# Kernel tuning notes

Hardware: AMD Instinct MI355X
Metric: run time of the kernel (lower is better)

Reference implementation:

```python
import jax, jax.numpy as jnp
import numpy as np
import math

D_MODEL = 1024
N_HEADS = 16
D_K = D_MODEL // N_HEADS
D_FF = 4096
B = 2
S = 2048
LN_EPS = 1e-3  # Keras LayerNormalization default


def setup_inputs() -> dict:
    key = jax.random.key(0)
    ks = jax.random.split(key, 16)
    s = 0.02
    inp = {
        "x": jax.random.normal(ks[0], (B, S, D_MODEL), dtype=jnp.float32),
        "weights": jax.random.uniform(ks[1], (B, S), dtype=jnp.float32),
        # attention projections (Dense: y = x @ W + b)
        "Wq": jax.random.normal(ks[2], (D_MODEL, D_MODEL), jnp.float32) * s,
        "bq": jnp.zeros((D_MODEL,), jnp.float32),
        "Wk": jax.random.normal(ks[3], (D_MODEL, D_MODEL), jnp.float32) * s,
        "bk": jnp.zeros((D_MODEL,), jnp.float32),
        "Wv": jax.random.normal(ks[4], (D_MODEL, D_MODEL), jnp.float32) * s,
        "bv": jnp.zeros((D_MODEL,), jnp.float32),
        "Wo": jax.random.normal(ks[5], (D_MODEL, D_MODEL), jnp.float32) * s,
        "bo": jnp.zeros((D_MODEL,), jnp.float32),
        # FFN
        "W1": jax.random.normal(ks[6], (D_MODEL, D_FF), jnp.float32) * s,
        "b1": jnp.zeros((D_FF,), jnp.float32),
        "W2": jax.random.normal(ks[7], (D_FF, D_MODEL), jnp.float32) * s,
        "b2": jnp.zeros((D_MODEL,), jnp.float32),
        # layer norms
        "g1": jnp.ones((D_MODEL,), jnp.float32),
        "be1": jnp.zeros((D_MODEL,), jnp.float32),
        "g2": jnp.ones((D_MODEL,), jnp.float32),
        "be2": jnp.zeros((D_MODEL,), jnp.float32),
    }
    return inp


def _layer_norm(x, gamma, beta):
    mu = jnp.mean(x, axis=-1, keepdims=True)
    var = jnp.mean(jnp.square(x - mu), axis=-1, keepdims=True)
    return (x - mu) * jax.lax.rsqrt(var + LN_EPS) * gamma + beta


def _block(x, weights, Wq, bq, Wk, bk, Wv, bv, Wo, bo, W1, b1, W2, b2, g1, be1, g2, be2):
    b, s, _ = x.shape
    # projections -> (B, H, S, d_k)
    def split_heads(y):
        return y.reshape(b, s, N_HEADS, D_K).transpose(0, 2, 1, 3)
    Q = split_heads(x @ Wq + bq)
    K = split_heads(x @ Wk + bk)
    V = split_heads(x @ Wv + bv)
    scores = jnp.einsum("bhqd,bhkd->bhqk", Q, K) / math.sqrt(D_K)
    log_w = jnp.log(weights + 1e-20)[:, None, None, :]  # (B,1,1,S)
    attn = jax.nn.softmax(scores + log_w, axis=-1)
    out = jnp.einsum("bhqk,bhkd->bhqd", attn, V)
    out = out.transpose(0, 2, 1, 3).reshape(b, s, D_MODEL)
    attn_out = out @ Wo + bo
    h = _layer_norm(x + attn_out, g1, be1)
    ffn = jax.nn.relu(h @ W1 + b1) @ W2 + b2
    return _layer_norm(h + ffn, g2, be2)


def reference(x, weights, Wq, bq, Wk, bk, Wv, bv, Wo, bo, W1, b1, W2, b2, g1, be1, g2, be2):
    return _block(x, weights, Wq, bq, Wk, bk, Wv, bv, Wo, bo, W1, b1, W2, b2, g1, be1, g2, be2)
```

## Files before the change

kernel.cpp:

```cpp
#include <hip/hip_runtime.h>
#include <cstdint>
#include <cstddef>

#define DM 1024
#define NH 16
#define DKH 64
#define DFF 4096
#define NB 2
#define SQL 2048
#define MROWS (NB * SQL)
#define QKVN 3072

typedef __attribute__((ext_vector_type(8))) __bf16 bf16x8;
typedef __attribute__((ext_vector_type(8))) short short8;
typedef __attribute__((ext_vector_type(4))) float f32x4;

__device__ __forceinline__ unsigned short f2bf(float f) {
    unsigned u = __float_as_uint(f);
    u += 0x7fffu + ((u >> 16) & 1u);
    return (unsigned short)(u >> 16);
}
__device__ __forceinline__ float bf2f(unsigned short u) {
    return __uint_as_float(((unsigned)u) << 16);
}
__device__ __forceinline__ bf16x8 ldfrag(const unsigned short* p) {
    return __builtin_bit_cast(bf16x8, *(const short8*)p);
}
__device__ __forceinline__ void gl_lds16(const void* g, void* lds) {
    __builtin_amdgcn_global_load_lds(
        (const __attribute__((address_space(1))) unsigned int*)g,
        (__attribute__((address_space(3))) unsigned int*)lds, 16, 0, 0);
}
#define MFMA16(a, b, c) __builtin_amdgcn_mfma_f32_16x16x32_bf16(a, b, c, 0, 0, 0)

__global__ __launch_bounds__(256) void cast_f32_bf16(const float* __restrict__ in,
                                                     unsigned short* __restrict__ out, int n) {
    int i = (blockIdx.x * 256 + threadIdx.x) * 4;
    if (i < n) {
        float4 v = *(const float4*)&in[i];
        ushort4 o;
        o.x = f2bf(v.x); o.y = f2bf(v.y); o.z = f2bf(v.z); o.w = f2bf(v.w);
        *(ushort4*)&out[i] = o;
    }
}

__global__ __launch_bounds__(256) void transpose_f32_bf16(const float* __restrict__ in,
                                                          unsigned short* __restrict__ out,
                                                          int K, int N, float scale) {
    __shared__ float tile[32][33];
    const int n0 = blockIdx.x * 32, k0 = blockIdx.y * 32;
    const int tx = threadIdx.x & 31, ty = threadIdx.x >> 5;
#pragma unroll
    for (int i = 0; i < 32; i += 8)
        tile[ty + i][tx] = in[(size_t)(k0 + ty + i) * N + n0 + tx];
    __syncthreads();
#pragma unroll
    for (int i = 0; i < 32; i += 8)
        out[(size_t)(n0 + ty + i) * K + k0 + tx] = f2bf(tile[tx][ty + i] * scale);
}

__global__ __launch_bounds__(256) void vt_transpose(const unsigned short* __restrict__ qkv,
                                                    unsigned short* __restrict__ vt) {
    __shared__ unsigned short tile[32][33];
    const int s0 = blockIdx.x * 32, d0 = blockIdx.y * 32, bh = blockIdx.z;
    const int b = bh >> 4, h = bh & 15;
    const int tx = threadIdx.x & 31, ty = threadIdx.x >> 5;
#pragma unroll
    for (int i = 0; i < 32; i += 8)
        tile[ty + i][tx] = qkv[(size_t)(b * SQL + s0 + ty + i) * QKVN + 2048 + h * DKH + d0 + tx];
    __syncthreads();
#pragma unroll
    for (int i = 0; i < 32; i += 8)
        vt[(size_t)bh * DKH * SQL + (size_t)(d0 + ty + i) * SQL + s0 + tx] = tile[tx][ty + i];
}

__global__ __launch_bounds__(256) void logw_kernel(const float* __restrict__ w,
                                                   float* __restrict__ lw, int n) {
    int i = blockIdx.x * 256 + threadIdx.x;
    if (i < n) lw[i] = logf(w[i] + 1e-20f);
}

__global__ __launch_bounds__(256) void bqkv_kernel(const float* __restrict__ bq,
                                                   const float* __restrict__ bk,
                                                   const float* __restrict__ bv,
                                                   float* __restrict__ out) {
    int i = blockIdx.x * 256 + threadIdx.x;
    if (i < QKVN)
        out[i] = i < 1024 ? bq[i] * 0.125f : (i < 2048 ? bk[i - 1024] : bv[i - 2048]);
}

template <int BN, bool RELU, bool OUT_BF16>
__global__ __launch_bounds__(256) void gemm_kernel(const unsigned short* __restrict__ A,
                                                   const unsigned short* __restrict__ Wt,
                                                   const float* __restrict__ bias,
                                                   void* __restrict__ outp,
                                                   int M, int N, int K) {
    constexpr int NT = BN / 32;
    __shared__ unsigned short As[128 * 64];
    __shared__ unsigned short Bs[BN * 64];
    const int tid = threadIdx.x;
    const int wave = tid >> 6, lane = tid & 63;
    const int col16 = lane & 15, quad = lane >> 4;
    const int lrow = lane >> 3, sblk = (lane & 7) ^ (lrow & 7);
    const int m0 = blockIdx.y * 128, n0 = blockIdx.x * BN;
    const int wm = (wave >> 1) * 64, wn = (wave & 1) * (BN / 2);

    f32x4 acc[4][NT] = {};

    for (int k0 = 0; k0 < K; k0 += 64) {
        __syncthreads();
#pragma unroll
        for (int c = wave; c < 16; c += 4)
            gl_lds16(&A[(size_t)(m0 + c * 8 + lrow) * K + k0 + sblk * 8], &As[c * 512]);
#pragma unroll
        for (int c = wave; c < BN / 8; c += 4)
            gl_lds16(&Wt[(size_t)(n0 + c * 8 + lrow) * K + k0 + sblk * 8], &Bs[c * 512]);
        __syncthreads();
#pragma unroll
        for (int kk8 = 0; kk8 < 8; kk8 += 4) {
            bf16x8 af[4], bfr[NT];
#pragma unroll
            for (int t = 0; t < 4; ++t) {
                int R = wm + t * 16 + col16;
                af[t] = ldfrag(&As[R * 64 + (((kk8 + quad) ^ (R & 7)) << 3)]);
            }
#pragma unroll
            for (int t = 0; t < NT; ++t) {
                int R = wn + t * 16 + col16;
                bfr[t] = ldfrag(&Bs[R * 64 + (((kk8 + quad) ^ (R & 7)) << 3)]);
            }
#pragma unroll
            for (int mt = 0; mt < 4; ++mt)
#pragma unroll
                for (int nt = 0; nt < NT; ++nt)
                    acc[mt][nt] = MFMA16(af[mt], bfr[nt], acc[mt][nt]);
        }
    }

#pragma unroll
    for (int mt = 0; mt < 4; ++mt)
#pragma unroll
        for (int nt = 0; nt < NT; ++nt) {
            int col = n0 + wn + nt * 16 + col16;
            float bv = bias[col];
#pragma unroll
            for (int r = 0; r < 4; ++r) {
                int row = m0 + wm + mt * 16 + quad * 4 + r;
                float v = acc[mt][nt][r] + bv;
                if (RELU) v = fmaxf(v, 0.f);
                if (OUT_BF16)
                    ((unsigned short*)outp)[(size_t)row * N + col] = f2bf(v);
                else
                    ((float*)outp)[(size_t)row * N + col] = v;
            }
        }
}

__global__ __launch_bounds__(256) void flash_kernel(const unsigned short* __restrict__ qkv,
                                                    const unsigned short* __restrict__ vt,
                                                    const float* __restrict__ logw,
                                                    unsigned short* __restrict__ outb) {
    __shared__ unsigned short Ks[64 * 64];
    __shared__ unsigned short Vt[64 * 64];
    __shared__ unsigned short Ps[4][16][72];
    __shared__ float lws[64];

    const int tid = threadIdx.x, wave = tid >> 6, lane = tid & 63;
    const int col16 = lane & 15, quad = lane >> 4;
    const int lrow = lane >> 3, sblk = (lane & 7) ^ (lrow & 7);
    const int bh = blockIdx.y, b = bh >> 4, h = bh & 15;
    const int q0 = blockIdx.x * 64;

    const unsigned short* Kg = qkv + (size_t)b * SQL * QKVN + 1024 + h * DKH;
    const unsigned short* Vg = vt + (size_t)bh * DKH * SQL;

    bf16x8 qf[2];
    {
        const unsigned short* qrow = qkv + (size_t)(b * SQL + q0 + wave * 16 + col16) * QKVN + h * DKH;
        qf[0] = ldfrag(qrow + quad * 8);
        qf[1] = ldfrag(qrow + 32 + quad * 8);
    }
    bf16x8 ones;
    {
        short8 o8 = {0x3f80, 0x3f80, 0x3f80, 0x3f80, 0x3f80, 0x3f80, 0x3f80, 0x3f80};
        ones = __builtin_bit_cast(bf16x8, o8);
    }

    f32x4 o[4] = {};
    f32x4 lacc = {};

    for (int kt = 0; kt < SQL; kt += 64) {
        __syncthreads();
#pragma unroll
        for (int c = wave; c < 8; c += 4) {
            gl_lds16(&Kg[(size_t)(kt + c * 8 + lrow) * QKVN + sblk * 8], &Ks[c * 512]);
            gl_lds16(&Vg[(size_t)(c * 8 + lrow) * SQL + kt + sblk * 8], &Vt[c * 512]);
        }
        if (tid < 64) lws[tid] = logw[b * SQL + kt + tid];
        __syncthreads();

        float pv[4][4];
#pragma unroll
        for (int nt = 0; nt < 4; ++nt) {
            int R = nt * 16 + col16;
            f32x4 s4 = {};
            s4 = MFMA16(qf[0], ldfrag(&Ks[R * 64 + ((quad ^ (R & 7)) << 3)]), s4);
            s4 = MFMA16(qf[1], ldfrag(&Ks[R * 64 + (((4 + quad) ^ (R & 7)) << 3)]), s4);
            float lw = lws[R];
#pragma unroll
            for (int r = 0; r < 4; ++r) pv[nt][r] = __expf(s4[r] + lw);
        }
#pragma unroll
        for (int nt = 0; nt < 4; ++nt)
#pragma unroll
            for (int r = 0; r < 4; ++r)
                Ps[wave][quad * 4 + r][nt * 16 + col16] = f2bf(pv[nt][r]);
        __syncthreads();

#pragma unroll
        for (int kk8 = 0; kk8 < 8; kk8 += 4) {
            bf16x8 psf = ldfrag(&Ps[wave][col16][(kk8 + quad) << 3]);
            lacc = MFMA16(ones, psf, lacc);
#pragma unroll
            for (int dt = 0; dt < 4; ++dt) {
                int R = dt * 16 + col16;
                bf16x8 vf = ldfrag(&Vt[R * 64 + (((kk8 + quad) ^ (R & 7)) << 3)]);
                o[dt] = MFMA16(vf, psf, o[dt]);
            }
        }
    }

    const float rl = 1.0f / lacc[0];
    const int qrow = b * SQL + q0 + wave * 16 + col16;
#pragma unroll
    for (int dt = 0; dt < 4; ++dt) {
        ushort4 h4;
        h4.x = f2bf(o[dt][0] * rl);
        h4.y = f2bf(o[dt][1] * rl);
        h4.z = f2bf(o[dt][2] * rl);
        h4.w = f2bf(o[dt][3] * rl);
        *(ushort4*)&outb[(size_t)qrow * DM + h * DKH + dt * 16 + quad * 4] = h4;
    }
}

__global__ __launch_bounds__(256) void ln1_kernel(const float* __restrict__ x,
                                                  const float* __restrict__ delta,
                                                  const float* __restrict__ g,
                                                  const float* __restrict__ be,
                                                  float* __restrict__ hf,
                                                  unsigned short* __restrict__ hb) {
    const int row = blockIdx.x, tid = threadIdx.x;
    float4 xv = *(const float4*)&x[(size_t)row * DM + tid * 4];
    float4 dv = *(const float4*)&delta[(size_t)row * DM + tid * 4];
    float v[4] = {xv.x + dv.x, xv.y + dv.y, xv.z + dv.z, xv.w + dv.w};
    float s = v[0] + v[1] + v[2] + v[3];
    float ss = v[0] * v[0] + v[1] * v[1] + v[2] * v[2] + v[3] * v[3];
#pragma unroll
    for (int m = 1; m < 64; m <<= 1) { s += __shfl_xor(s, m); ss += __shfl_xor(ss, m); }
    __shared__ float sb[4], ssb[4];
    if ((tid & 63) == 0) { sb[tid >> 6] = s; ssb[tid >> 6] = ss; }
    __syncthreads();
    s = sb[0] + sb[1] + sb[2] + sb[3];
    ss = ssb[0] + ssb[1] + ssb[2] + ssb[3];
    float mu = s * (1.f / DM);
    float var = fmaxf(ss * (1.f / DM) - mu * mu, 0.f);
    float rs = rsqrtf(var + 1e-3f);
#pragma unroll
    for (int i = 0; i < 4; ++i) {
        int c = tid * 4 + i;
        float y = (v[i] - mu) * rs * g[c] + be[c];
        hf[(size_t)row * DM + c] = y;
        hb[(size_t)row * DM + c] = f2bf(y);
    }
}

__global__ __launch_bounds__(256) void ln2_kernel(const float* __restrict__ hf,
                                                  const float* __restrict__ delta,
                                                  const float* __restrict__ g,
                                                  const float* __restrict__ be,
                                                  float* __restrict__ outp) {
    const int row = blockIdx.x, tid = threadIdx.x;
    float4 hv = *(const float4*)&hf[(size_t)row * DM + tid * 4];
    float4 dv = *(const float4*)&delta[(size_t)row * DM + tid * 4];
    float v[4] = {hv.x + dv.x, hv.y + dv.y, hv.z + dv.z, hv.w + dv.w};
    float s = v[0] + v[1] + v[2] + v[3];
    float ss = v[0] * v[0] + v[1] * v[1] + v[2] * v[2] + v[3] * v[3];
#pragma unroll
    for (int m = 1; m < 64; m <<= 1) { s += __shfl_xor(s, m); ss += __shfl_xor(ss, m); }
    __shared__ float sb[4], ssb[4];
    if ((tid & 63) == 0) { sb[tid >> 6] = s; ssb[tid >> 6] = ss; }
    __syncthreads();
    s = sb[0] + sb[1] + sb[2] + sb[3];
    ss = ssb[0] + ssb[1] + ssb[2] + ssb[3];
    float mu = s * (1.f / DM);
    float var = fmaxf(ss * (1.f / DM) - mu * mu, 0.f);
    float rs = rsqrtf(var + 1e-3f);
    float4 ov;
    ov.x = (v[0] - mu) * rs * g[tid * 4 + 0] + be[tid * 4 + 0];
    ov.y = (v[1] - mu) * rs * g[tid * 4 + 1] + be[tid * 4 + 1];
    ov.z = (v[2] - mu) * rs * g[tid * 4 + 2] + be[tid * 4 + 2];
    ov.w = (v[3] - mu) * rs * g[tid * 4 + 3] + be[tid * 4 + 3];
    *(float4*)&outp[(size_t)row * DM + tid * 4] = ov;
}

extern "C" void kernel_launch(void* const* d_in, const int* in_sizes, int n_in,
                              void* d_out, int out_size, void* d_ws, size_t ws_size,
                              hipStream_t stream) {
    const float* x   = (const float*)d_in[0];
    const float* wts = (const float*)d_in[1];
    const float* Wq  = (const float*)d_in[2];
    const float* bq  = (const float*)d_in[3];
    const float* Wk  = (const float*)d_in[4];
    const float* bk  = (const float*)d_in[5];
    const float* Wv  = (const float*)d_in[6];
    const float* bv  = (const float*)d_in[7];
    const float* Wo  = (const float*)d_in[8];
    const float* bo  = (const float*)d_in[9];
    const float* W1  = (const float*)d_in[10];
    const float* b1  = (const float*)d_in[11];
    const float* W2  = (const float*)d_in[12];
    const float* b2  = (const float*)d_in[13];
    const float* g1  = (const float*)d_in[14];
    const float* be1 = (const float*)d_in[15];
    const float* g2  = (const float*)d_in[16];
    const float* be2 = (const float*)d_in[17];

    char* ws = (char*)d_ws;
    const size_t MB = 1u << 20;
    unsigned short* qkv_bf  = (unsigned short*)(ws + 0 * MB);
    unsigned short* vt      = (unsigned short*)(ws + 24 * MB);
    float* attnproj         = (float*)(ws + 0 * MB);
    unsigned short* ffn1_bf = (unsigned short*)(ws + 0 * MB);
    unsigned short* x_bf    = (unsigned short*)(ws + 32 * MB);
    unsigned short* wqkv_t  = (unsigned short*)(ws + 40 * MB);
    unsigned short* Wo_t    = (unsigned short*)(ws + 46 * MB);
    unsigned short* W1_t    = (unsigned short*)(ws + 48 * MB);
    unsigned short* W2_t    = (unsigned short*)(ws + 56 * MB);
    float* ffn2             = (float*)(ws + 32 * MB);
    unsigned short* attn_bf = (unsigned short*)(ws + 64 * MB);
    float* h_f32            = (float*)(ws + 72 * MB);
    unsigned short* h_bf    = (unsigned short*)(ws + 88 * MB);
    float* bqkv             = (float*)(ws + 96 * MB);
    float* logw             = (float*)(ws + 96 * MB + 16384);

    cast_f32_bf16<<<(MROWS * DM) / 1024, 256, 0, stream>>>(x, x_bf, MROWS * DM);
    transpose_f32_bf16<<<dim3(32, 32), 256, 0, stream>>>(Wq, wqkv_t, DM, DM, 0.125f);
    transpose_f32_bf16<<<dim3(32, 32), 256, 0, stream>>>(Wk, wqkv_t + (size_t)1024 * DM, DM, DM, 1.f);
    transpose_f32_bf16<<<dim3(32, 32), 256, 0, stream>>>(Wv, wqkv_t + (size_t)2048 * DM, DM, DM, 1.f);
    transpose_f32_bf16<<<dim3(32, 32), 256, 0, stream>>>(Wo, Wo_t, DM, DM, 1.f);
    transpose_f32_bf16<<<dim3(128, 32), 256, 0, stream>>>(W1, W1_t, DM, DFF, 1.f);
    transpose_f32_bf16<<<dim3(32, 128), 256, 0, stream>>>(W2, W2_t, DFF, DM, 1.f);
    bqkv_kernel<<<12, 256, 0, stream>>>(bq, bk, bv, bqkv);
    logw_kernel<<<(MROWS + 255) / 256, 256, 0, stream>>>(wts, logw, MROWS);

    gemm_kernel<128, false, true><<<dim3(QKVN / 128, MROWS / 128), 256, 0, stream>>>(
        x_bf, wqkv_t, bqkv, qkv_bf, MROWS, QKVN, DM);

    vt_transpose<<<dim3(SQL / 32, DKH / 32, NB * NH), 256, 0, stream>>>(qkv_bf, vt);
    flash_kernel<<<dim3(SQL / 64, NB * NH), 256, 0, stream>>>(qkv_bf, vt, logw, attn_bf);

    gemm_kernel<64, false, false><<<dim3(DM / 64, MROWS / 128), 256, 0, stream>>>(
        attn_bf, Wo_t, bo, attnproj, MROWS, DM, DM);
    ln1_kernel<<<MROWS, 256, 0, stream>>>(x, attnproj, g1, be1, h_f32, h_bf);

    gemm_kernel<128, true, true><<<dim3(DFF / 128, MROWS / 128), 256, 0, stream>>>(
        h_bf, W1_t, b1, ffn1_bf, MROWS, DFF, DM);
    gemm_kernel<64, false, false><<<dim3(DM / 64, MROWS / 128), 256, 0, stream>>>(
        ffn1_bf, W2_t, b2, ffn2, MROWS, DM, DFF);
    ln2_kernel<<<MROWS, 256, 0, stream>>>(h_f32, ffn2, g2, be2, (float*)d_out);
}
```

Baseline: 398.8 us.

## Split attention KV range and narrow GEMMs along K to raise occupancy

The flash attention kernel now splits each query tile's key range into two halves as separate blocks. It writes unnormalized fp32 partial outputs and row sums, which a new combine kernel adds and normalizes into bf16. The Wo and W2 GEMMs (N=1024) now use a 2-way split-K. Each split writes its own fp32 partial buffer, and the LayerNorm kernels add both partials. The goal is more blocks on a GPU with many CUs. The cost is extra memory traffic for the partial buffers, one more kernel launch, and a workspace rearrangement that moves the W2 transpose later.

```diff
diff --git a/kernel.cpp b/kernel.cpp
--- a/kernel.cpp
+++ b/kernel.cpp
@@ -89,7 +89,7 @@
         out[i] = i < 1024 ? bq[i] * 0.125f : (i < 2048 ? bk[i - 1024] : bv[i - 2048]);
 }
 
-template <int BN, bool RELU, bool OUT_BF16>
+template <int BN, bool RELU, bool OUT_BF16, int KSPL>
 __global__ __launch_bounds__(256) void gemm_kernel(const unsigned short* __restrict__ A,
                                                    const unsigned short* __restrict__ Wt,
                                                    const float* __restrict__ bias,
@@ -104,10 +104,12 @@
     const int lrow = lane >> 3, sblk = (lane & 7) ^ (lrow & 7);
     const int m0 = blockIdx.y * 128, n0 = blockIdx.x * BN;
     const int wm = (wave >> 1) * 64, wn = (wave & 1) * (BN / 2);
+    const int kbeg = (KSPL > 1) ? blockIdx.z * (K / KSPL) : 0;
+    const int kend = kbeg + K / KSPL;
 
     f32x4 acc[4][NT] = {};
 
-    for (int k0 = 0; k0 < K; k0 += 64) {
+    for (int k0 = kbeg; k0 < kend; k0 += 64) {
         __syncthreads();
 #pragma unroll
         for (int c = wave; c < 16; c += 4)
@@ -137,12 +139,13 @@
         }
     }
 
+    float* outf = (float*)outp + ((KSPL > 1) ? (size_t)blockIdx.z * M * N : 0);
 #pragma unroll
     for (int mt = 0; mt < 4; ++mt)
 #pragma unroll
         for (int nt = 0; nt < NT; ++nt) {
             int col = n0 + wn + nt * 16 + col16;
-            float bv = bias[col];
+            float bv = (KSPL == 1 || blockIdx.z == 0) ? bias[col] : 0.f;
 #pragma unroll
             for (int r = 0; r < 4; ++r) {
                 int row = m0 + wm + mt * 16 + quad * 4 + r;
@@ -151,7 +154,7 @@
                 if (OUT_BF16)
                     ((unsigned short*)outp)[(size_t)row * N + col] = f2bf(v);
                 else
-                    ((float*)outp)[(size_t)row * N + col] = v;
+                    outf[(size_t)row * N + col] = v;
             }
         }
 }
@@ -159,7 +162,8 @@
 __global__ __launch_bounds__(256) void flash_kernel(const unsigned short* __restrict__ qkv,
                                                     const unsigned short* __restrict__ vt,
                                                     const float* __restrict__ logw,
-                                                    unsigned short* __restrict__ outb) {
+                                                    float* __restrict__ po,
+                                                    float* __restrict__ pl) {
     __shared__ unsigned short Ks[64 * 64];
     __shared__ unsigned short Vt[64 * 64];
     __shared__ unsigned short Ps[4][16][72];
@@ -170,13 +174,15 @@
     const int lrow = lane >> 3, sblk = (lane & 7) ^ (lrow & 7);
     const int bh = blockIdx.y, b = bh >> 4, h = bh & 15;
     const int q0 = blockIdx.x * 64;
+    const int split = blockIdx.z;
 
     const unsigned short* Kg = qkv + (size_t)b * SQL * QKVN + 1024 + h * DKH;
     const unsigned short* Vg = vt + (size_t)bh * DKH * SQL;
 
     bf16x8 qf[2];
     {
-        const unsigned short* qrow = qkv + (size_t)(b * SQL + q0 + wave * 16 + col16) * QKVN + h * DKH;
+        const unsigned short* qrow =
+            qkv + (size_t)(b * SQL + q0 + wave * 16 + col16) * QKVN + h * DKH;
         qf[0] = ldfrag(qrow + quad * 8);
         qf[1] = ldfrag(qrow + 32 + quad * 8);
     }
@@ -189,7 +195,7 @@
     f32x4 o[4] = {};
     f32x4 lacc = {};
 
-    for (int kt = 0; kt < SQL; kt += 64) {
+    for (int kt = split * (SQL / 2); kt < (split + 1) * (SQL / 2); kt += 64) {
         __syncthreads();
 #pragma unroll
         for (int c = wave; c < 8; c += 4) {
@@ -230,29 +236,47 @@
         }
     }
 
-    const float rl = 1.0f / lacc[0];
-    const int qrow = b * SQL + q0 + wave * 16 + col16;
+    const size_t prow = (size_t)(split * 32 + bh) * SQL + q0 + wave * 16 + col16;
 #pragma unroll
     for (int dt = 0; dt < 4; ++dt) {
-        ushort4 h4;
-        h4.x = f2bf(o[dt][0] * rl);
-        h4.y = f2bf(o[dt][1] * rl);
-        h4.z = f2bf(o[dt][2] * rl);
-        h4.w = f2bf(o[dt][3] * rl);
-        *(ushort4*)&outb[(size_t)qrow * DM + h * DKH + dt * 16 + quad * 4] = h4;
-    }
+        float4 v4 = {o[dt][0], o[dt][1], o[dt][2], o[dt][3]};
+        *(float4*)&po[prow * 64 + dt * 16 + quad * 4] = v4;
+    }
+    if (quad == 0) pl[prow] = lacc[0];
+}
+
+__global__ __launch_bounds__(256) void combine_kernel(const float* __restrict__ po,
+                                                      const float* __restrict__ pl,
+                                                      unsigned short* __restrict__ attn_bf) {
+    const int gid = blockIdx.x * 256 + threadIdx.x;
+    const int t = gid & 15;
+    const int row = gid >> 4;
+    const int bh = row >> 11, q = row & 2047;
+    const int b = bh >> 4, h = bh & 15;
+    float4 a = *(const float4*)&po[(size_t)row * 64 + t * 4];
+    float4 c = *(const float4*)&po[(size_t)(row + 65536) * 64 + t * 4];
+    float rl = 1.f / (pl[row] + pl[row + 65536]);
+    ushort4 o;
+    o.x = f2bf((a.x + c.x) * rl);
+    o.y = f2bf((a.y + c.y) * rl);
+    o.z = f2bf((a.z + c.z) * rl);
+    o.w = f2bf((a.w + c.w) * rl);
+    *(ushort4*)&attn_bf[(size_t)(b * SQL + q) * DM + h * DKH + t * 4] = o;
 }
 
 __global__ __launch_bounds__(256) void ln1_kernel(const float* __restrict__ x,
-                                                  const float* __restrict__ delta,
+                                                  const float* __restrict__ d0,
+                                                  const float* __restrict__ d1,
                                                   const float* __restrict__ g,
                                                   const float* __restrict__ be,
                                                   float* __restrict__ hf,
                                                   unsigned short* __restrict__ hb) {
     const int row = blockIdx.x, tid = threadIdx.x;
     float4 xv = *(const float4*)&x[(size_t)row * DM + tid * 4];
-    float4 dv = *(const float4*)&delta[(size_t)row * DM + tid * 4];
-    float v[4] = {xv.x + dv.x, xv.y + dv.y, xv.z + dv.z, xv.w + dv.w};
+    float4 av = *(const float4*)&d0[(size_t)row * DM + tid * 4];
+    float4 bv = *(const float4*)&d1[(size_t)row * DM + tid * 4];
+    float v[4] = {xv.x + av.x + bv.x, xv.y + av.y + bv.y, xv.z + av.z + bv.z,
+                  xv.w + av.w + bv.w};
     float s = v[0] + v[1] + v[2] + v[3];
     float ss = v[0] * v[0] + v[1] * v[1] + v[2] * v[2] + v[3] * v[3];
 #pragma unroll
@@ -275,14 +299,17 @@
 }
 
 __global__ __launch_bounds__(256) void ln2_kernel(const float* __restrict__ hf,
-                                                  const float* __restrict__ delta,
+                                                  const float* __restrict__ d0,
+                                                  const float* __restrict__ d1,
                                                   const float* __restrict__ g,
                                                   const float* __restrict__ be,
                                                   float* __restrict__ outp) {
     const int row = blockIdx.x, tid = threadIdx.x;
     float4 hv = *(const float4*)&hf[(size_t)row * DM + tid * 4];
-    float4 dv = *(const float4*)&delta[(size_t)row * DM + tid * 4];
-    float v[4] = {hv.x + dv.x, hv.y + dv.y, hv.z + dv.z, hv.w + dv.w};
+    float4 av = *(const float4*)&d0[(size_t)row * DM + tid * 4];
+    float4 bv = *(const float4*)&d1[(size_t)row * DM + tid * 4];
+    float v[4] = {hv.x + av.x + bv.x, hv.y + av.y + bv.y, hv.z + av.z + bv.z,
+                  hv.w + av.w + bv.w};
     float s = v[0] + v[1] + v[2] + v[3];
     float ss = v[0] * v[0] + v[1] * v[1] + v[2] * v[2] + v[3] * v[3];
 #pragma unroll
@@ -329,19 +356,21 @@
     const size_t MB = 1u << 20;
     unsigned short* qkv_bf  = (unsigned short*)(ws + 0 * MB);
     unsigned short* vt      = (unsigned short*)(ws + 24 * MB);
-    float* attnproj         = (float*)(ws + 0 * MB);
-    unsigned short* ffn1_bf = (unsigned short*)(ws + 0 * MB);
     unsigned short* x_bf    = (unsigned short*)(ws + 32 * MB);
     unsigned short* wqkv_t  = (unsigned short*)(ws + 40 * MB);
     unsigned short* Wo_t    = (unsigned short*)(ws + 46 * MB);
     unsigned short* W1_t    = (unsigned short*)(ws + 48 * MB);
-    unsigned short* W2_t    = (unsigned short*)(ws + 56 * MB);
+    float* po               = (float*)(ws + 64 * MB);
+    unsigned short* W2_t    = (unsigned short*)(ws + 88 * MB);
+    float* pl               = (float*)(ws + 98 * MB);
+    float* bqkv             = (float*)(ws + 98 * MB + 0x80000);
+    float* logw             = (float*)(ws + 98 * MB + 0x88000);
+    unsigned short* attn_bf = (unsigned short*)(ws + 32 * MB);
+    float* attnproj         = (float*)(ws + 0 * MB);
+    float* h_f32            = (float*)(ws + 64 * MB);
+    unsigned short* h_bf    = (unsigned short*)(ws + 80 * MB);
+    unsigned short* ffn1_bf = (unsigned short*)(ws + 0 * MB);
     float* ffn2             = (float*)(ws + 32 * MB);
-    unsigned short* attn_bf = (unsigned short*)(ws + 64 * MB);
-    float* h_f32            = (float*)(ws + 72 * MB);
-    unsigned short* h_bf    = (unsigned short*)(ws + 88 * MB);
-    float* bqkv             = (float*)(ws + 96 * MB);
-    float* logw             = (float*)(ws + 96 * MB + 16384);
 
     cast_f32_bf16<<<(MROWS * DM) / 1024, 256, 0, stream>>>(x, x_bf, MROWS * DM);
     transpose_f32_bf16<<<dim3(32, 32), 256, 0, stream>>>(Wq, wqkv_t, DM, DM, 0.125f);
@@ -349,23 +378,27 @@
     transpose_f32_bf16<<<dim3(32, 32), 256, 0, stream>>>(Wv, wqkv_t + (size_t)2048 * DM, DM, DM, 1.f);
     transpose_f32_bf16<<<dim3(32, 32), 256, 0, stream>>>(Wo, Wo_t, DM, DM, 1.f);
     transpose_f32_bf16<<<dim3(128, 32), 256, 0, stream>>>(W1, W1_t, DM, DFF, 1.f);
-    transpose_f32_bf16<<<dim3(32, 128), 256, 0, stream>>>(W2, W2_t, DFF, DM, 1.f);
     bqkv_kernel<<<12, 256, 0, stream>>>(bq, bk, bv, bqkv);
     logw_kernel<<<(MROWS + 255) / 256, 256, 0, stream>>>(wts, logw, MROWS);
 
-    gemm_kernel<128, false, true><<<dim3(QKVN / 128, MROWS / 128), 256, 0, stream>>>(
+    gemm_kernel<128, false, true, 1><<<dim3(QKVN / 128, MROWS / 128), 256, 0, stream>>>(
         x_bf, wqkv_t, bqkv, qkv_bf, MROWS, QKVN, DM);
 
     vt_transpose<<<dim3(SQL / 32, DKH / 32, NB * NH), 256, 0, stream>>>(qkv_bf, vt);
-    flash_kernel<<<dim3(SQL / 64, NB * NH), 256, 0, stream>>>(qkv_bf, vt, logw, attn_bf);
-
-    gemm_kernel<64, false, false><<<dim3(DM / 64, MROWS / 128), 256, 0, stream>>>(
+    flash_kernel<<<dim3(SQL / 64, NB * NH, 2), 256, 0, stream>>>(qkv_bf, vt, logw, po, pl);
+    combine_kernel<<<(32 * 2048 * 16) / 256, 256, 0, stream>>>(po, pl, attn_bf);
+
+    transpose_f32_bf16<<<dim3(32, 128), 256, 0, stream>>>(W2, W2_t, DFF, DM, 1.f);
+
+    gemm_kernel<64, false, false, 2><<<dim3(DM / 64, MROWS / 128, 2), 256, 0, stream>>>(
         attn_bf, Wo_t, bo, attnproj, MROWS, DM, DM);
-    ln1_kernel<<<MROWS, 256, 0, stream>>>(x, attnproj, g1, be1, h_f32, h_bf);
-
-    gemm_kernel<128, true, true><<<dim3(DFF / 128, MROWS / 128), 256, 0, stream>>>(
+    ln1_kernel<<<MROWS, 256, 0, stream>>>(x, attnproj, attnproj + (size_t)MROWS * DM,
+                                          g1, be1, h_f32, h_bf);
+
+    gemm_kernel<128, true, true, 1><<<dim3(DFF / 128, MROWS / 128), 256, 0, stream>>>(
         h_bf, W1_t, b1, ffn1_bf, MROWS, DFF, DM);
-    gemm_kernel<64, false, false><<<dim3(DM / 64, MROWS / 128), 256, 0, stream>>>(
+    gemm_kernel<64, false, false, 2><<<dim3(DM / 64, MROWS / 128, 2), 256, 0, stream>>>(
         ffn1_bf, W2_t, b2, ffn2, MROWS, DM, DFF);
-    ln2_kernel<<<MROWS, 256, 0, stream>>>(h_f32, ffn2, g2, be2, (float*)d_out);
-}
+    ln2_kernel<<<MROWS, 256, 0, stream>>>(h_f32, ffn2, ffn2 + (size_t)MROWS * DM,
+                                          g2, be2, (float*)d_out);
+}
```

After: 382.6 us. 4.1% less time.
